# Kernel optimization log

Measured on AMD Instinct MI355X. Metric: run time of the kernel, lower is better.

## Reference

```python
import jax, jax.numpy as jnp
import numpy as np

TAU = 0.5  # init tau
EPS = 1e-8  # F.cosine_similarity eps


def setup_inputs() -> dict:
    key = jax.random.key(0)
    k1, k2 = jax.random.split(key)
    N, D, NUM_CLASSES = 4096, 1024, 128
    layer_embeds = jax.random.normal(k1, (N, D), dtype=jnp.float32)
    y_true = jax.random.randint(k2, (N,), 0, NUM_CLASSES, dtype=jnp.int64)
    return {"layer_embeds": layer_embeds, "y_true": y_true}


def reference(layer_embeds, y_true):
    N = layer_embeds.shape[0]
    # batched cosine similarity, scaled like the original: (cos + 1) * 0.5 * tau
    norms = jnp.maximum(jnp.linalg.norm(layer_embeds, axis=1), EPS)  # [N]
    cos = (layer_embeds @ layer_embeds.T) / (norms[:, None] * norms[None, :])  # [N, N]
    S = (cos + 1.0) * 0.5 * TAU

    same = y_true[:, None] == y_true[None, :]  # [N, N]
    eye = jnp.eye(N, dtype=bool)
    pos_mask = same & ~eye            # same-label pairs, j != i
    neg_mask = ~same                  # different-label pairs (diag excluded since same there)

    # column 0: first positive (in j order), else stays 0
    has_pos = pos_mask.any(axis=1)
    first_pos = jnp.argmax(pos_mask, axis=1)
    pos_val = jnp.where(has_pos, S[jnp.arange(N), first_pos], 0.0)  # [N]

    # negatives fill columns 1.. in j order: col = 1 + (#negatives with j' < j)
    negi = neg_mask.astype(jnp.int32)
    col = 1 + jnp.cumsum(negi, axis=1) - negi  # [N, N]
    W = 2 * N  # pad one dummy column for non-negative entries
    cols = jnp.where(neg_mask, col, W - 1)
    rows = jnp.broadcast_to(jnp.arange(N)[:, None], (N, N))
    loss_temp = jnp.zeros((N, W), dtype=jnp.float32)
    loss_temp = loss_temp.at[rows, cols].set(jnp.where(neg_mask, S, 0.0))
    loss_temp = loss_temp.at[:, 0].set(pos_val)
    loss_temp = loss_temp[:, : 2 * N - 1]  # [N, 2N-1], matches torch buffer

    # -log_softmax, take column 0, sum over rows, divide by N
    lse = jax.nn.logsumexp(loss_temp, axis=1)  # [N]
    loss = jnp.sum(lse - loss_temp[:, 0]) / N
    return loss
```

## Files before the change

kernel.cpp:

```cpp
#include <hip/hip_runtime.h>
#include <hip/hip_bf16.h>
#include <math.h>

#define NN 4096
#define DD 1024
#define NCLS 128
#define TAU 0.5f
#define EPSV 1e-8f

typedef __bf16 bf16;
typedef __bf16 bf16x8 __attribute__((ext_vector_type(8)));
typedef __bf16 bf16x4 __attribute__((ext_vector_type(4)));
typedef float f32x4 __attribute__((ext_vector_type(4)));

__device__ __forceinline__ void gl2lds16(const void* g, void* l) {
    __builtin_amdgcn_global_load_lds(
        (const __attribute__((address_space(1))) void*)g,
        (__attribute__((address_space(3))) void*)l,
        16, 0, 0);
}

__global__ __launch_bounds__(256) void k_norm_cast(const float* __restrict__ X,
                                                   bf16* __restrict__ Xn,
                                                   float* __restrict__ rsum) {
    int w = threadIdx.x >> 6, lane = threadIdx.x & 63;
    int row = blockIdx.x * 4 + w;
    const float* xr = X + (size_t)row * DD;
    float4 v[4];
    float ss = 0.f;
#pragma unroll
    for (int c = 0; c < 4; ++c) {
        v[c] = *(const float4*)(xr + c * 256 + lane * 4);
        ss += v[c].x * v[c].x + v[c].y * v[c].y + v[c].z * v[c].z + v[c].w * v[c].w;
    }
#pragma unroll
    for (int m = 1; m < 64; m <<= 1) ss += __shfl_xor(ss, m, 64);
    float rn = 1.f / fmaxf(sqrtf(ss), EPSV);
    if (lane == 0) rsum[row] = 0.f;
#pragma unroll
    for (int c = 0; c < 4; ++c) {
        bf16x4 o;
        o.x = (bf16)(v[c].x * rn);
        o.y = (bf16)(v[c].y * rn);
        o.z = (bf16)(v[c].z * rn);
        o.w = (bf16)(v[c].w * rn);
        *(bf16x4*)(Xn + (size_t)row * DD + c * 256 + lane * 4) = o;
    }
}

__global__ __launch_bounds__(1024) void k_classes(const int* __restrict__ y,
                                                  int* __restrict__ cnt,
                                                  int* __restrict__ mn1,
                                                  int* __restrict__ mn2) {
    __shared__ int sc[NCLS], s1[NCLS], s2[NCLS];
    int t = threadIdx.x;
    if (t < NCLS) { sc[t] = 0; s1[t] = 0x7fffffff; s2[t] = 0x7fffffff; }
    __syncthreads();
    int yv[4];
#pragma unroll
    for (int k = 0; k < 4; ++k) {
        int i = t + k * 1024;
        yv[k] = y[i];
        atomicAdd(&sc[yv[k]], 1);
        atomicMin(&s1[yv[k]], i);
    }
    __syncthreads();
#pragma unroll
    for (int k = 0; k < 4; ++k) {
        int i = t + k * 1024;
        if (s1[yv[k]] != i) atomicMin(&s2[yv[k]], i);
    }
    __syncthreads();
    if (t < NCLS) { cnt[t] = sc[t]; mn1[t] = s1[t]; mn2[t] = s2[t]; }
}

__global__ __launch_bounds__(256) void k_posval(const bf16* __restrict__ Xn,
                                                const int* __restrict__ y,
                                                const int* __restrict__ cnt,
                                                const int* __restrict__ mn1,
                                                const int* __restrict__ mn2,
                                                float* __restrict__ posv) {
    int w = threadIdx.x >> 6, lane = threadIdx.x & 63;
    int i = blockIdx.x * 4 + w;
    int c = y[i];
    float pv = 0.f;
    if (cnt[c] >= 2) {
        int fp = (mn1[c] == i) ? mn2[c] : mn1[c];
        const bf16* xi = Xn + (size_t)i * DD;
        const bf16* xf = Xn + (size_t)fp * DD;
        float dot = 0.f;
#pragma unroll
        for (int cc = 0; cc < 2; ++cc) {
            bf16x8 a = *(const bf16x8*)(xi + cc * 512 + lane * 8);
            bf16x8 b = *(const bf16x8*)(xf + cc * 512 + lane * 8);
#pragma unroll
            for (int e = 0; e < 8; ++e) dot += (float)a[e] * (float)b[e];
        }
#pragma unroll
        for (int m = 1; m < 64; m <<= 1) dot += __shfl_xor(dot, m, 64);
        pv = (dot + 1.f) * (0.5f * TAU);
    }
    if (lane == 0) posv[i] = pv;
}

__global__ __launch_bounds__(256) void k_gemm(const bf16* __restrict__ Xn,
                                              const int* __restrict__ y,
                                              float* __restrict__ rowsum) {
    __shared__ __align__(16) bf16 As[128 * 32];
    __shared__ __align__(16) bf16 Bs[128 * 32];
    __shared__ int yA[128], yB[128];

    int id = blockIdx.x;
    float ff = sqrtf((float)(8 * id + 1));
    int bj = (int)((ff - 1.f) * 0.5f);
    if (bj * (bj + 1) / 2 > id) bj--;
    if ((bj + 1) * (bj + 2) / 2 <= id) bj++;
    int bi = id - bj * (bj + 1) / 2;
    const int rowA0 = bi * 128;
    const int rowB0 = bj * 128;
    const bool diag = (bi == bj);

    const int tid = threadIdx.x;
    if (tid < 128) yA[tid] = y[rowA0 + tid];
    else           yB[tid - 128] = y[rowB0 + tid - 128];

    const int lane = tid & 63;
    const int w = tid >> 6;
    const int wm = w & 1, wn = w >> 1;
    const int lr = lane >> 4, lc = lane & 15;

    f32x4 acc[4][4];
#pragma unroll
    for (int i = 0; i < 4; ++i)
#pragma unroll
        for (int j = 0; j < 4; ++j) acc[i][j] = (f32x4){0.f, 0.f, 0.f, 0.f};

    const int r = tid >> 2;
    const int g = tid & 3;
    const int kg = g ^ ((r >> 1) & 3);
    const bf16* gA0 = Xn + (size_t)(rowA0 + r) * DD + kg * 8;
    const bf16* gA1 = gA0 + (size_t)64 * DD;
    const bf16* gB0 = Xn + (size_t)(rowB0 + r) * DD + kg * 8;
    const bf16* gB1 = gB0 + (size_t)64 * DD;
    bf16* lA0 = As + tid * 8;
    bf16* lA1 = As + 64 * 32 + tid * 8;
    bf16* lB0 = Bs + tid * 8;
    bf16* lB1 = Bs + 64 * 32 + tid * 8;

    const int sw = (lc >> 1) & 3;

    for (int k0 = 0; k0 < DD; k0 += 32) {
        __syncthreads();
        gl2lds16(gA0 + k0, lA0);
        gl2lds16(gA1 + k0, lA1);
        gl2lds16(gB0 + k0, lB0);
        gl2lds16(gB1 + k0, lB1);
        __syncthreads();

        bf16x8 af[4], bfr[4];
#pragma unroll
        for (int mt = 0; mt < 4; ++mt)
            af[mt] = *(const bf16x8*)(As + (wm * 64 + mt * 16 + lc) * 32 + ((lr ^ sw) * 8));
#pragma unroll
        for (int nt = 0; nt < 4; ++nt)
            bfr[nt] = *(const bf16x8*)(Bs + (wn * 64 + nt * 16 + lc) * 32 + ((lr ^ sw) * 8));
#pragma unroll
        for (int mt = 0; mt < 4; ++mt)
#pragma unroll
            for (int nt = 0; nt < 4; ++nt)
                acc[mt][nt] = __builtin_amdgcn_mfma_f32_16x16x32_bf16(
                    af[mt], bfr[nt], acc[mt][nt], 0, 0, 0);
    }

    int ycol[4];
#pragma unroll
    for (int nt = 0; nt < 4; ++nt) ycol[nt] = yB[wn * 64 + nt * 16 + lc];
    float colacc[4] = {0.f, 0.f, 0.f, 0.f};
#pragma unroll
    for (int mt = 0; mt < 4; ++mt) {
#pragma unroll
        for (int rr = 0; rr < 4; ++rr) {
            int rloc = wm * 64 + mt * 16 + lr * 4 + rr;
            int yrow = yA[rloc];
            float s = 0.f;
#pragma unroll
            for (int nt = 0; nt < 4; ++nt) {
                float Sv = (acc[mt][nt][rr] + 1.f) * (0.5f * TAU);
                float e = (ycol[nt] != yrow) ? __expf(Sv) : 0.f;
                s += e;
                colacc[nt] += e;
            }
            s += __shfl_xor(s, 1, 16);
            s += __shfl_xor(s, 2, 16);
            s += __shfl_xor(s, 4, 16);
            s += __shfl_xor(s, 8, 16);
            if (lc == 0) atomicAdd(&rowsum[rowA0 + rloc], s);
        }
    }
    if (!diag) {
#pragma unroll
        for (int nt = 0; nt < 4; ++nt) {
            float cs = colacc[nt];
            cs += __shfl_xor(cs, 16, 64);
            cs += __shfl_xor(cs, 32, 64);
            if (lane < 16) atomicAdd(&rowsum[rowB0 + wn * 64 + nt * 16 + lane], cs);
        }
    }
}

__global__ __launch_bounds__(1024) void k_finalize(const float* __restrict__ rowsum,
                                                   const float* __restrict__ posv,
                                                   const int* __restrict__ y,
                                                   const int* __restrict__ cnt,
                                                   float* __restrict__ out) {
    int t = threadIdx.x;
    float acc = 0.f;
#pragma unroll
    for (int k = 0; k < 4; ++k) {
        int i = t + k * 1024;
        float pv = posv[i];
        float tot = rowsum[i] + __expf(pv) + (float)(NN - 2 + cnt[y[i]]);
        acc += logf(tot) - pv;
    }
#pragma unroll
    for (int m = 1; m < 64; m <<= 1) acc += __shfl_xor(acc, m, 64);
    __shared__ float wsum[16];
    int w = t >> 6, lane = t & 63;
    if (lane == 0) wsum[w] = acc;
    __syncthreads();
    if (t == 0) {
        float s = 0.f;
#pragma unroll
        for (int q = 0; q < 16; ++q) s += wsum[q];
        *out = s / (float)NN;
    }
}

extern "C" void kernel_launch(void* const* d_in, const int* in_sizes, int n_in,
                              void* d_out, int out_size, void* d_ws, size_t ws_size,
                              hipStream_t stream) {
    const float* X = (const float*)d_in[0];
    const int* y = (const int*)d_in[1];
    float* out = (float*)d_out;

    char* ws = (char*)d_ws;
    bf16* Xn     = (bf16*)ws;
    float* rsum  = (float*)(ws + 8 * 1024 * 1024);
    float* posv  = (float*)(ws + 8 * 1024 * 1024 + 16 * 1024);
    int* cnt     = (int*)(ws + 8 * 1024 * 1024 + 32 * 1024);
    int* mn1     = (int*)(ws + 8 * 1024 * 1024 + 32 * 1024 + 512);
    int* mn2     = (int*)(ws + 8 * 1024 * 1024 + 32 * 1024 + 1024);

    k_norm_cast<<<dim3(NN / 4), 256, 0, stream>>>(X, Xn, rsum);
    k_classes<<<dim3(1), 1024, 0, stream>>>(y, cnt, mn1, mn2);
    k_posval<<<dim3(NN / 4), 256, 0, stream>>>(Xn, y, cnt, mn1, mn2, posv);
    k_gemm<<<dim3(528), 256, 0, stream>>>(Xn, y, rsum);
    k_finalize<<<dim3(1), 1024, 0, stream>>>(rsum, posv, y, cnt, out);
}
```

Measured before the change: 106.5 us.

## Fuse class stats into prep, positives into GEMM epilogue, finalize via last-block

```diff
diff --git a/kernel.cpp b/kernel.cpp
--- a/kernel.cpp
+++ b/kernel.cpp
@@ -7,6 +7,7 @@
 #define NCLS 128
 #define TAU 0.5f
 #define EPSV 1e-8f
+#define NB_GEMM 528
 
 typedef __bf16 bf16;
 typedef __bf16 bf16x8 __attribute__((ext_vector_type(8)));
@@ -20,11 +21,46 @@
         16, 0, 0);
 }
 
-__global__ __launch_bounds__(256) void k_norm_cast(const float* __restrict__ X,
-                                                   bf16* __restrict__ Xn,
-                                                   float* __restrict__ rsum) {
-    int w = threadIdx.x >> 6, lane = threadIdx.x & 63;
-    int row = blockIdx.x * 4 + w;
+__global__ __launch_bounds__(256) void k_prep(const float* __restrict__ X,
+                                              const int* __restrict__ y,
+                                              bf16* __restrict__ Xn,
+                                              float* __restrict__ rsum,
+                                              float* __restrict__ posv,
+                                              int* __restrict__ cnt,
+                                              int* __restrict__ fpos,
+                                              int* __restrict__ ctr) {
+    const int t = threadIdx.x;
+    if (blockIdx.x == 0) {
+        __shared__ int sc[NCLS], s1[NCLS], s2[NCLS];
+        if (t < NCLS) { sc[t] = 0; s1[t] = 0x7fffffff; s2[t] = 0x7fffffff; }
+        if (t == 0) *ctr = 0;
+        __syncthreads();
+        int yv[16];
+#pragma unroll
+        for (int k = 0; k < 16; ++k) {
+            int i = t + k * 256;
+            yv[k] = y[i];
+            atomicAdd(&sc[yv[k]], 1);
+            atomicMin(&s1[yv[k]], i);
+        }
+        __syncthreads();
+#pragma unroll
+        for (int k = 0; k < 16; ++k) {
+            int i = t + k * 256;
+            if (s1[yv[k]] != i) atomicMin(&s2[yv[k]], i);
+        }
+        __syncthreads();
+#pragma unroll
+        for (int k = 0; k < 16; ++k) {
+            int i = t + k * 256;
+            int c = yv[k];
+            fpos[i] = (sc[c] >= 2) ? (s1[c] == i ? s2[c] : s1[c]) : -1;
+        }
+        if (t < NCLS) cnt[t] = sc[t];
+        return;
+    }
+    const int w = t >> 6, lane = t & 63;
+    const int row = (blockIdx.x - 1) * 4 + w;
     const float* xr = X + (size_t)row * DD;
     float4 v[4];
     float ss = 0.f;
@@ -36,7 +72,7 @@
 #pragma unroll
     for (int m = 1; m < 64; m <<= 1) ss += __shfl_xor(ss, m, 64);
     float rn = 1.f / fmaxf(sqrtf(ss), EPSV);
-    if (lane == 0) rsum[row] = 0.f;
+    if (lane == 0) { rsum[row] = 0.f; posv[row] = 0.f; }
 #pragma unroll
     for (int c = 0; c < 4; ++c) {
         bf16x4 o;
@@ -48,67 +84,19 @@
     }
 }
 
-__global__ __launch_bounds__(1024) void k_classes(const int* __restrict__ y,
-                                                  int* __restrict__ cnt,
-                                                  int* __restrict__ mn1,
-                                                  int* __restrict__ mn2) {
-    __shared__ int sc[NCLS], s1[NCLS], s2[NCLS];
-    int t = threadIdx.x;
-    if (t < NCLS) { sc[t] = 0; s1[t] = 0x7fffffff; s2[t] = 0x7fffffff; }
-    __syncthreads();
-    int yv[4];
-#pragma unroll
-    for (int k = 0; k < 4; ++k) {
-        int i = t + k * 1024;
-        yv[k] = y[i];
-        atomicAdd(&sc[yv[k]], 1);
-        atomicMin(&s1[yv[k]], i);
-    }
-    __syncthreads();
-#pragma unroll
-    for (int k = 0; k < 4; ++k) {
-        int i = t + k * 1024;
-        if (s1[yv[k]] != i) atomicMin(&s2[yv[k]], i);
-    }
-    __syncthreads();
-    if (t < NCLS) { cnt[t] = sc[t]; mn1[t] = s1[t]; mn2[t] = s2[t]; }
-}
-
-__global__ __launch_bounds__(256) void k_posval(const bf16* __restrict__ Xn,
-                                                const int* __restrict__ y,
-                                                const int* __restrict__ cnt,
-                                                const int* __restrict__ mn1,
-                                                const int* __restrict__ mn2,
-                                                float* __restrict__ posv) {
-    int w = threadIdx.x >> 6, lane = threadIdx.x & 63;
-    int i = blockIdx.x * 4 + w;
-    int c = y[i];
-    float pv = 0.f;
-    if (cnt[c] >= 2) {
-        int fp = (mn1[c] == i) ? mn2[c] : mn1[c];
-        const bf16* xi = Xn + (size_t)i * DD;
-        const bf16* xf = Xn + (size_t)fp * DD;
-        float dot = 0.f;
-#pragma unroll
-        for (int cc = 0; cc < 2; ++cc) {
-            bf16x8 a = *(const bf16x8*)(xi + cc * 512 + lane * 8);
-            bf16x8 b = *(const bf16x8*)(xf + cc * 512 + lane * 8);
-#pragma unroll
-            for (int e = 0; e < 8; ++e) dot += (float)a[e] * (float)b[e];
-        }
-#pragma unroll
-        for (int m = 1; m < 64; m <<= 1) dot += __shfl_xor(dot, m, 64);
-        pv = (dot + 1.f) * (0.5f * TAU);
-    }
-    if (lane == 0) posv[i] = pv;
-}
-
 __global__ __launch_bounds__(256) void k_gemm(const bf16* __restrict__ Xn,
                                               const int* __restrict__ y,
-                                              float* __restrict__ rowsum) {
+                                              const int* __restrict__ fpos,
+                                              const int* __restrict__ cnt,
+                                              float* __restrict__ rowsum,
+                                              float* __restrict__ posv,
+                                              int* __restrict__ ctr,
+                                              float* __restrict__ out) {
     __shared__ __align__(16) bf16 As[128 * 32];
     __shared__ __align__(16) bf16 Bs[128 * 32];
-    __shared__ int yA[128], yB[128];
+    __shared__ int yA[128], yB[128], fA[128], fB[128];
+    __shared__ int isLast;
+    __shared__ float wred[4];
 
     int id = blockIdx.x;
     float ff = sqrtf((float)(8 * id + 1));
@@ -121,8 +109,8 @@
     const bool diag = (bi == bj);
 
     const int tid = threadIdx.x;
-    if (tid < 128) yA[tid] = y[rowA0 + tid];
-    else           yB[tid - 128] = y[rowB0 + tid - 128];
+    if (tid < 128) { yA[tid] = y[rowA0 + tid]; fA[tid] = fpos[rowA0 + tid]; }
+    else { yB[tid - 128] = y[rowB0 + tid - 128]; fB[tid - 128] = fpos[rowB0 + tid - 128]; }
 
     const int lane = tid & 63;
     const int w = tid >> 6;
@@ -172,20 +160,32 @@
                     af[mt], bfr[nt], acc[mt][nt], 0, 0, 0);
     }
 
-    int ycol[4];
-#pragma unroll
-    for (int nt = 0; nt < 4; ++nt) ycol[nt] = yB[wn * 64 + nt * 16 + lc];
+    int cloc[4], ycol[4], fcol[4];
+    bool pcol[4];
+#pragma unroll
+    for (int nt = 0; nt < 4; ++nt) {
+        cloc[nt] = wn * 64 + nt * 16 + lc;
+        ycol[nt] = yB[cloc[nt]];
+        fcol[nt] = fB[cloc[nt]];
+        pcol[nt] = ((unsigned)(fcol[nt] - rowA0) < 128u);
+    }
     float colacc[4] = {0.f, 0.f, 0.f, 0.f};
 #pragma unroll
     for (int mt = 0; mt < 4; ++mt) {
 #pragma unroll
         for (int rr = 0; rr < 4; ++rr) {
             int rloc = wm * 64 + mt * 16 + lr * 4 + rr;
+            int rglob = rowA0 + rloc;
             int yrow = yA[rloc];
+            int fprow = fA[rloc];
+            bool prow = ((unsigned)(fprow - rowB0) < 128u);
             float s = 0.f;
 #pragma unroll
             for (int nt = 0; nt < 4; ++nt) {
                 float Sv = (acc[mt][nt][rr] + 1.f) * (0.5f * TAU);
+                int cg = rowB0 + cloc[nt];
+                if (prow && cg == fprow) atomicExch(&posv[rglob], Sv);
+                if (pcol[nt] && fcol[nt] == rglob) atomicExch(&posv[cg], Sv);
                 float e = (ycol[nt] != yrow) ? __expf(Sv) : 0.f;
                 s += e;
                 colacc[nt] += e;
@@ -194,7 +194,7 @@
             s += __shfl_xor(s, 2, 16);
             s += __shfl_xor(s, 4, 16);
             s += __shfl_xor(s, 8, 16);
-            if (lc == 0) atomicAdd(&rowsum[rowA0 + rloc], s);
+            if (lc == 0) atomicAdd(&rowsum[rglob], s);
         }
     }
     if (!diag) {
@@ -206,34 +206,28 @@
             if (lane < 16) atomicAdd(&rowsum[rowB0 + wn * 64 + nt * 16 + lane], cs);
         }
     }
-}
-
-__global__ __launch_bounds__(1024) void k_finalize(const float* __restrict__ rowsum,
-                                                   const float* __restrict__ posv,
-                                                   const int* __restrict__ y,
-                                                   const int* __restrict__ cnt,
-                                                   float* __restrict__ out) {
-    int t = threadIdx.x;
-    float acc = 0.f;
-#pragma unroll
-    for (int k = 0; k < 4; ++k) {
-        int i = t + k * 1024;
-        float pv = posv[i];
-        float tot = rowsum[i] + __expf(pv) + (float)(NN - 2 + cnt[y[i]]);
-        acc += logf(tot) - pv;
-    }
-#pragma unroll
-    for (int m = 1; m < 64; m <<= 1) acc += __shfl_xor(acc, m, 64);
-    __shared__ float wsum[16];
-    int w = t >> 6, lane = t & 63;
-    if (lane == 0) wsum[w] = acc;
+
+    __threadfence();
     __syncthreads();
-    if (t == 0) {
-        float s = 0.f;
-#pragma unroll
-        for (int q = 0; q < 16; ++q) s += wsum[q];
-        *out = s / (float)NN;
-    }
+    if (tid == 0) isLast = (atomicAdd(ctr, 1) == NB_GEMM - 1);
+    __syncthreads();
+    if (!isLast) return;
+    __threadfence();
+
+    float acc2 = 0.f;
+#pragma unroll
+    for (int k = 0; k < 16; ++k) {
+        int i = tid + k * 256;
+        float rs = atomicAdd(&rowsum[i], 0.0f);
+        float pv = atomicAdd(&posv[i], 0.0f);
+        float tot = rs + __expf(pv) + (float)(NN - 2 + cnt[y[i]]);
+        acc2 += logf(tot) - pv;
+    }
+#pragma unroll
+    for (int m = 1; m < 64; m <<= 1) acc2 += __shfl_xor(acc2, m, 64);
+    if ((tid & 63) == 0) wred[tid >> 6] = acc2;
+    __syncthreads();
+    if (tid == 0) *out = (wred[0] + wred[1] + wred[2] + wred[3]) / (float)NN;
 }
 
 extern "C" void kernel_launch(void* const* d_in, const int* in_sizes, int n_in,
@@ -244,16 +238,13 @@
     float* out = (float*)d_out;
 
     char* ws = (char*)d_ws;
-    bf16* Xn     = (bf16*)ws;
-    float* rsum  = (float*)(ws + 8 * 1024 * 1024);
-    float* posv  = (float*)(ws + 8 * 1024 * 1024 + 16 * 1024);
-    int* cnt     = (int*)(ws + 8 * 1024 * 1024 + 32 * 1024);
-    int* mn1     = (int*)(ws + 8 * 1024 * 1024 + 32 * 1024 + 512);
-    int* mn2     = (int*)(ws + 8 * 1024 * 1024 + 32 * 1024 + 1024);
-
-    k_norm_cast<<<dim3(NN / 4), 256, 0, stream>>>(X, Xn, rsum);
-    k_classes<<<dim3(1), 1024, 0, stream>>>(y, cnt, mn1, mn2);
-    k_posval<<<dim3(NN / 4), 256, 0, stream>>>(Xn, y, cnt, mn1, mn2, posv);
-    k_gemm<<<dim3(528), 256, 0, stream>>>(Xn, y, rsum);
-    k_finalize<<<dim3(1), 1024, 0, stream>>>(rsum, posv, y, cnt, out);
-}
+    bf16* Xn    = (bf16*)ws;
+    float* rsum = (float*)(ws + 8 * 1024 * 1024);
+    float* posv = (float*)(ws + 8 * 1024 * 1024 + 16 * 1024);
+    int* cnt    = (int*)(ws + 8 * 1024 * 1024 + 32 * 1024);
+    int* ctr    = (int*)(ws + 8 * 1024 * 1024 + 32 * 1024 + 512);
+    int* fpos   = (int*)(ws + 8 * 1024 * 1024 + 36 * 1024);
+
+    k_prep<<<dim3(NN / 4 + 1), 256, 0, stream>>>(X, y, Xn, rsum, posv, cnt, fpos, ctr);
+    k_gemm<<<dim3(NB_GEMM), 256, 0, stream>>>(Xn, y, fpos, cnt, rsum, posv, ctr, out);
+}
```

After: 157.2 us. 47.6% more time.
